# Performance work log

Measured on AMD Instinct MI355X. Metric: run time of the kernel, lower is better.

Reference implementation:

```python
import jax, jax.numpy as jnp
import numpy as np

B, F, T, D, O = 8192, 512, 64, 6, 128
N_INTERNAL = 2 ** D - 1  # 63
N_LEAVES = 2 ** D        # 64


def smooth_step(t):
    tc = jnp.clip(t, -0.5, 0.5)
    return -2.0 * tc ** 3 + 1.5 * tc + 0.5


def setup_inputs() -> dict:
    key = jax.random.key(0)
    k1, k2, k3, k4 = jax.random.split(key, 4)
    x = jax.random.normal(k1, (B, F), dtype=jnp.float32)
    # Stacked per-node Linear weights in BFS (heap) order: node i -> row i.
    W_nodes = jax.random.normal(k2, (N_INTERNAL, F, T), dtype=jnp.float32) * (1.0 / np.sqrt(F))
    b_nodes = jax.random.normal(k3, (N_INTERNAL, T), dtype=jnp.float32) * 0.01
    # Per-leaf mixing weight [out_features, num_trees], leaves in BFS order.
    W_leaf = jax.random.normal(k4, (N_LEAVES, O, T), dtype=jnp.float32)
    return {"x": x, "W_nodes": W_nodes, "b_nodes": b_nodes, "W_leaf": W_leaf}


def reference(x, W_nodes, b_nodes, W_leaf):
    n_internal = W_nodes.shape[0]
    depth = int(np.log2(n_internal + 1))
    # All internal-node gates in one stacked GEMM: [B, n_internal, T]
    s = smooth_step(jnp.einsum('bf,nft->bnt', x, W_nodes) + b_nodes[None, :, :])
    b, _, t = s.shape
    prob = jnp.ones((b, 1, t), dtype=s.dtype)  # root prob
    start = 0
    for lvl in range(depth):
        width = 2 ** lvl
        s_l = s[:, start:start + width]  # [B, width, T], nodes at this level
        start += width
        # node local j -> children local 2j (left, prob*s) and 2j+1 (right, prob*(1-s))
        prob = jnp.stack([prob * s_l, prob * (1.0 - s_l)], axis=2).reshape(b, 2 * width, t)
    # prob: [B, n_leaves, T]; mix per-leaf, per-tree weights -> [B, O]
    out = jnp.einsum('blt,lot->bo', prob, W_leaf)
    return out
```

## Files before the change

kernel.cpp:

```cpp
#include <hip/hip_runtime.h>
#include <hip/hip_fp16.h>

#define BATCH 8192
#define FDIM  512
#define NTREE 64
#define NODES 63
#define ODIM  128
#define NJ    (NODES*NTREE)
#define NJP   4096
#define K2    4096

typedef _Float16 f16;
typedef _Float16 f16x8 __attribute__((ext_vector_type(8)));
typedef float    f32x4 __attribute__((ext_vector_type(4)));

#define XH_OFF   0
#define XH_SZ    ((size_t)BATCH*FDIM*2)
#define WNH_OFF  (XH_OFF + XH_SZ)
#define WNH_SZ   ((size_t)NJP*FDIM*2)
#define WLT_OFF  (WNH_OFF + WNH_SZ)
#define WLT_SZ   ((size_t)ODIM*K2*2)
#define SP_OFF   (WLT_OFF + WLT_SZ)
#define SP_SZ    ((size_t)BATCH*NJP*2)
#define WS_NEEDED (SP_OFF + SP_SZ)

__device__ __forceinline__ float smooth_step_f(float t) {
    float tc = fminf(fmaxf(t, -0.5f), 0.5f);
    return fmaf(tc, fmaf(-2.0f * tc, tc, 1.5f), 0.5f);
}

__device__ __forceinline__ void async16(const void* g, void* l) {
    __builtin_amdgcn_global_load_lds((__attribute__((address_space(1))) void*)g,
                                     (__attribute__((address_space(3))) void*)l,
                                     16, 0, 0);
}

__device__ __forceinline__ int sw_off(int row, int g) {
    return ((row >> 3) * 512) + (((row & 7) * 8 + (g ^ (row & 7))) * 8);
}

__global__ void conv_x_kernel(const float* __restrict__ in, f16* __restrict__ out) {
    size_t i = ((size_t)blockIdx.x * blockDim.x + threadIdx.x) * 4;
    float4 v = *(const float4*)(in + i);
    f16* o = out + i;
    o[0] = (f16)v.x; o[1] = (f16)v.y; o[2] = (f16)v.z; o[3] = (f16)v.w;
}

__global__ void conv_wl_kernel(const float* __restrict__ in, f16* __restrict__ out) {
    const int l  = blockIdx.x;
    const int os = threadIdx.x >> 6;
    const int t  = threadIdx.x & 63;
    for (int oo = 0; oo < 32; ++oo) {
        int o = oo * 4 + os;
        out[(size_t)o * K2 + l * 64 + t] = (f16)in[(size_t)l * (ODIM * NTREE) + o * 64 + t];
    }
}

__global__ void conv_wn_kernel(const float* __restrict__ wn, f16* __restrict__ out) {
    const int n    = blockIdx.x;
    const int f0   = blockIdx.y * 64;
    const int lane = threadIdx.x & 63;
    const int w    = threadIdx.x >> 6;
    if (n == NODES) {
        #pragma unroll
        for (int jj = 0; jj < 16; ++jj) {
            int j = NJ + w * 16 + jj;
            out[(size_t)j * FDIM + f0 + lane] = (f16)0.0f;
        }
        return;
    }
    __shared__ float tile[64][65];
    const float* src = wn + (size_t)n * (FDIM * NTREE);
    #pragma unroll
    for (int i = 0; i < 16; ++i) {
        int fl = w * 16 + i;
        tile[fl][lane] = src[(size_t)(f0 + fl) * NTREE + lane];
    }
    __syncthreads();
    #pragma unroll
    for (int i = 0; i < 16; ++i) {
        int tr = w * 16 + i;
        out[(size_t)(n * 64 + tr) * FDIM + f0 + lane] = (f16)tile[lane][tr];
    }
}

__global__ __launch_bounds__(256, 3)
void gemm_nodes(const f16* __restrict__ xh, const f16* __restrict__ wnh,
                const float* __restrict__ bn, f16* __restrict__ s_out)
{
    __shared__ f16 SH[128 * 128];
    f16* Ash = SH;
    f16* Bsh = SH + 128 * 64;
    const int tid  = threadIdx.x;
    const int lane = tid & 63;
    const int w    = tid >> 6;
    const int wm   = w & 1;
    const int wn   = w >> 1;
    const int j0   = blockIdx.x * 128;
    const int row0 = blockIdx.y * 128;

    const int lr = lane >> 3;
    const int lg = (lane & 7) ^ lr;
    f32x4 acc[4][4] = {};

    for (int k0 = 0; k0 < FDIM; k0 += 64) {
        #pragma unroll
        for (int q = 0; q < 8; ++q) {
            int id = w * 8 + q;
            if (id < 16) {
                int r = id * 8 + lr;
                async16(xh + (size_t)(row0 + r) * FDIM + k0 + lg * 8, &Ash[id * 512 + lane * 8]);
            } else {
                int c = id - 16;
                int r = c * 8 + lr;
                async16(wnh + (size_t)(j0 + r) * FDIM + k0 + lg * 8, &Bsh[c * 512 + lane * 8]);
            }
        }
        __syncthreads();
        #pragma unroll
        for (int ks = 0; ks < 2; ++ks) {
            int g = ks * 4 + (lane >> 4);
            f16x8 bfr[4];
            #pragma unroll
            for (int tn = 0; tn < 4; ++tn) {
                int j = wn * 64 + tn * 16 + (lane & 15);
                bfr[tn] = *(const f16x8*)&Bsh[sw_off(j, g)];
            }
            #pragma unroll
            for (int tm = 0; tm < 4; ++tm) {
                int m = wm * 64 + tm * 16 + (lane & 15);
                f16x8 afr = *(const f16x8*)&Ash[sw_off(m, g)];
                #pragma unroll
                for (int tn = 0; tn < 4; ++tn)
                    acc[tm][tn] = __builtin_amdgcn_mfma_f32_16x16x32_f16(afr, bfr[tn], acc[tm][tn], 0, 0, 0);
            }
        }
        __syncthreads();
    }

    #pragma unroll
    for (int tn = 0; tn < 4; ++tn) {
        int col = wn * 64 + tn * 16 + (lane & 15);
        int j   = j0 + col;
        float bias = (j < NJ) ? bn[j] : 0.0f;
        #pragma unroll
        for (int tm = 0; tm < 4; ++tm) {
            #pragma unroll
            for (int r = 0; r < 4; ++r) {
                int row = wm * 64 + tm * 16 + (lane >> 4) * 4 + r;
                float v = acc[tm][tn][r] + bias;
                int scol = col ^ (((row >> 2) & 3) << 4);
                SH[row * 128 + scol] = (f16)smooth_step_f(v);
            }
        }
    }
    __syncthreads();
    const int4* shv = (const int4*)SH;
    #pragma unroll
    for (int it = 0; it < 8; ++it) {
        int idx = it * 256 + tid;
        int row = idx >> 4, c = idx & 15;
        int src = (row << 4) + (c ^ (((row >> 2) & 3) << 1));
        ((int4*)(s_out + (size_t)(row0 + row) * NJP + j0))[c] = shv[src];
    }
}

__global__ __launch_bounds__(256, 4)
void prob_kernel(f16* sp)
{
    __shared__ f16 stage[4 * 4096];
    const int lane = threadIdx.x & 63;
    const int w    = threadIdx.x >> 6;
    const size_t row = (size_t)blockIdx.x * 4 + w;
    f16* rp = sp + row * NJP;
    f16* L  = stage + w * 4096;

    #pragma unroll
    for (int c = 0; c < 8; ++c)
        async16(rp + c * 512 + lane * 8, L + c * 512 + lane * 8);
    __builtin_amdgcn_s_waitcnt(0);

    float pr[32];
    pr[0] = 1.0f;
    int base = 0;
    #pragma unroll
    for (int lvl = 0; lvl < 5; ++lvl) {
        const int width = 1 << lvl;
        float sl[16];
        #pragma unroll
        for (int i = 0; i < width; ++i)
            sl[i] = (float)L[(base + i) * 64 + lane];
        #pragma unroll
        for (int i = width - 1; i >= 0; --i) {
            float p = pr[i];
            pr[2 * i]     = p * sl[i];
            pr[2 * i + 1] = p * (1.0f - sl[i]);
        }
        base += width;
    }
    #pragma unroll
    for (int i = 0; i < 32; ++i) {
        float s5 = (float)L[(31 + i) * 64 + lane];
        float p  = pr[i];
        L[(2 * i) * 64 + lane]     = (f16)(p * s5);
        L[(2 * i + 1) * 64 + lane] = (f16)(p * (1.0f - s5));
    }
    const int4* ls = (const int4*)L;
    int4* gd = (int4*)rp;
    #pragma unroll
    for (int c = 0; c < 8; ++c)
        gd[c * 64 + lane] = ls[c * 64 + lane];
}

__global__ __launch_bounds__(256, 4)
void leaf_gemm(const f16* __restrict__ prob, const f16* __restrict__ wlt,
               float* __restrict__ out)
{
    __shared__ f16 Ash[2 * 16 * 64];
    __shared__ f16 Bsh[2 * 128 * 64];
    const int tid  = threadIdx.x;
    const int lane = tid & 63;
    const int w    = tid >> 6;
    const int row0 = blockIdx.x * 16;

    const int lr = lane >> 3;
    const int lg = (lane & 7) ^ lr;
    f32x4 acc[2] = {};

    for (int k0 = 0; k0 < K2; k0 += 128) {
        #pragma unroll
        for (int q = 0; q < 9; ++q) {
            int id = w * 9 + q;
            if (id < 4) {
                int t = id >> 1, c = id & 1;
                int r = c * 8 + lr;
                async16(prob + (size_t)(row0 + r) * NJP + k0 + t * 64 + lg * 8,
                        &Ash[t * 1024 + c * 512 + lane * 8]);
            } else {
                int e = id - 4;
                int t = e >> 4, c = e & 15;
                int o = c * 8 + lr;
                async16(wlt + (size_t)o * K2 + k0 + t * 64 + lg * 8,
                        &Bsh[t * 8192 + c * 512 + lane * 8]);
            }
        }
        __syncthreads();
        #pragma unroll
        for (int ks = 0; ks < 4; ++ks) {
            int t = ks >> 1;
            int g = (ks & 1) * 4 + (lane >> 4);
            int m = lane & 15;
            f16x8 afr = *(const f16x8*)&Ash[t * 1024 + sw_off(m, g)];
            #pragma unroll
            for (int tn = 0; tn < 2; ++tn) {
                int o = w * 32 + tn * 16 + (lane & 15);
                f16x8 bfr = *(const f16x8*)&Bsh[t * 8192 + sw_off(o, g)];
                acc[tn] = __builtin_amdgcn_mfma_f32_16x16x32_f16(afr, bfr, acc[tn], 0, 0, 0);
            }
        }
        __syncthreads();
    }
    #pragma unroll
    for (int tn = 0; tn < 2; ++tn) {
        int o = w * 32 + tn * 16 + (lane & 15);
        #pragma unroll
        for (int r = 0; r < 4; ++r) {
            int row = row0 + (lane >> 4) * 4 + r;
            out[(size_t)row * ODIM + o] = acc[tn][r];
        }
    }
}

#define ROWS 8
__global__ __launch_bounds__(256, 2)
void soft_tree_fallback(const float* __restrict__ x, const float* __restrict__ Wn,
                        const float* __restrict__ bn, const float* __restrict__ Wl,
                        float* __restrict__ out)
{
    __shared__ __half s_lds[ROWS][NODES][NTREE];
    const int lane = threadIdx.x & 63;
    const int w    = threadIdx.x >> 6;
    const long row0 = (long)blockIdx.x * ROWS;
    for (int n = w; n < NODES; n += 4) {
        const float* wp = Wn + ((long)n * FDIM) * NTREE + lane;
        const float* xp = x + row0 * FDIM;
        float acc[ROWS];
        #pragma unroll
        for (int r = 0; r < ROWS; ++r) acc[r] = 0.0f;
        #pragma unroll 8
        for (int f = 0; f < FDIM; ++f) {
            float wv = wp[(long)f * NTREE];
            #pragma unroll
            for (int r = 0; r < ROWS; ++r)
                acc[r] = fmaf(xp[r * FDIM + f], wv, acc[r]);
        }
        float bias = bn[n * NTREE + lane];
        #pragma unroll
        for (int r = 0; r < ROWS; ++r)
            s_lds[r][n][lane] = __float2half(smooth_step_f(acc[r] + bias));
    }
    __syncthreads();
    const int r0 = w * 2, r1 = w * 2 + 1;
    float pr0[64], pr1[64];
    {
        pr0[0] = 1.0f; pr1[0] = 1.0f;
        int base = 0;
        #pragma unroll
        for (int lvl = 0; lvl < 6; ++lvl) {
            const int width = 1 << lvl;
            #pragma unroll
            for (int i = width - 1; i >= 0; --i) {
                float sa = __half2float(s_lds[r0][base + i][lane]);
                float sb = __half2float(s_lds[r1][base + i][lane]);
                float pa = pr0[i], pb = pr1[i];
                pr0[2 * i] = pa * sa; pr0[2 * i + 1] = pa * (1.0f - sa);
                pr1[2 * i] = pb * sb; pr1[2 * i + 1] = pb * (1.0f - sb);
            }
            base += width;
        }
    }
    for (int o = 0; o < ODIM; ++o) {
        const float* wlp = Wl + (long)o * NTREE + lane;
        float c0 = 0.0f, c1 = 0.0f;
        #pragma unroll
        for (int l = 0; l < 64; ++l) {
            float wv = wlp[(long)l * (ODIM * NTREE)];
            c0 = fmaf(pr0[l], wv, c0);
            c1 = fmaf(pr1[l], wv, c1);
        }
        #pragma unroll
        for (int off = 32; off > 0; off >>= 1) {
            c0 += __shfl_xor(c0, off, 64);
            c1 += __shfl_xor(c1, off, 64);
        }
        if (lane == 0) {
            out[(row0 + r0) * ODIM + o] = c0;
            out[(row0 + r1) * ODIM + o] = c1;
        }
    }
}

extern "C" void kernel_launch(void* const* d_in, const int* in_sizes, int n_in,
                              void* d_out, int out_size, void* d_ws, size_t ws_size,
                              hipStream_t stream) {
    const float* x  = (const float*)d_in[0];
    const float* Wn = (const float*)d_in[1];
    const float* bn = (const float*)d_in[2];
    const float* Wl = (const float*)d_in[3];
    float* out = (float*)d_out;

    if (ws_size < WS_NEEDED) {
        soft_tree_fallback<<<BATCH / ROWS, 256, 0, stream>>>(x, Wn, bn, Wl, out);
        return;
    }

    f16* xh  = (f16*)((char*)d_ws + XH_OFF);
    f16* wnh = (f16*)((char*)d_ws + WNH_OFF);
    f16* wlt = (f16*)((char*)d_ws + WLT_OFF);
    f16* sp  = (f16*)((char*)d_ws + SP_OFF);

    conv_x_kernel <<<(BATCH * FDIM) / (256 * 4), 256, 0, stream>>>(x, xh);
    conv_wl_kernel<<<64, 256, 0, stream>>>(Wl, wlt);
    conv_wn_kernel<<<dim3(64, FDIM / 64), 256, 0, stream>>>(Wn, wnh);

    gemm_nodes<<<dim3(NJP / 128, BATCH / 128), 256, 0, stream>>>(xh, wnh, bn, sp);
    prob_kernel<<<BATCH / 4, 256, 0, stream>>>(sp);
    leaf_gemm<<<BATCH / 16, 256, 0, stream>>>(sp, wlt, out);
}
```

Before: 177.5 us.

## Store gate columns tree-major so prob and leaf kernels work from registers

Changes the node-weight column order from node-major (n*64+t) to tree-major (t*64+n), so each tree's 63 gates plus one pad are contiguous in the gate buffer. The prob kernel now has each lane load its tree's 64 gates as vector loads into registers and write the leaf probabilities back the same way, with no LDS staging. The leaf weight transpose is rebuilt to match the new K ordering, using an LDS tile and vectorized stores. The leaf GEMM drops its LDS tiles and syncs and reads MFMA fragments straight from global memory, which trades LDS traffic for more uncoalesced global loads and higher register pressure.

```diff
diff --git a/kernel.cpp b/kernel.cpp
--- a/kernel.cpp
+++ b/kernel.cpp
@@ -6,7 +6,6 @@
 #define NTREE 64
 #define NODES 63
 #define ODIM  128
-#define NJ    (NODES*NTREE)
 #define NJP   4096
 #define K2    4096
 
@@ -47,12 +46,25 @@
 }
 
 __global__ void conv_wl_kernel(const float* __restrict__ in, f16* __restrict__ out) {
-    const int l  = blockIdx.x;
-    const int os = threadIdx.x >> 6;
-    const int t  = threadIdx.x & 63;
-    for (int oo = 0; oo < 32; ++oo) {
-        int o = oo * 4 + os;
-        out[(size_t)o * K2 + l * 64 + t] = (f16)in[(size_t)l * (ODIM * NTREE) + o * 64 + t];
+    __shared__ f16 tile[64][72];
+    const int o    = blockIdx.x;
+    const int lane = threadIdx.x & 63;
+    const int w    = threadIdx.x >> 6;
+    #pragma unroll
+    for (int lc = 0; lc < 16; ++lc) {
+        int l = w * 16 + lc;
+        tile[lane][l] = (f16)in[(size_t)l * (ODIM * NTREE) + o * 64 + lane];
+    }
+    __syncthreads();
+    f16* orow = out + (size_t)o * K2;
+    #pragma unroll
+    for (int c = 0; c < 2; ++c) {
+        int idx = (threadIdx.x * 2 + c) * 8;
+        int t = idx >> 6, l = idx & 63;
+        f16x8 v;
+        #pragma unroll
+        for (int e = 0; e < 8; ++e) v[e] = tile[t][l + e];
+        *(f16x8*)(orow + idx) = v;
     }
 }
 
@@ -63,9 +75,9 @@
     const int w    = threadIdx.x >> 6;
     if (n == NODES) {
         #pragma unroll
-        for (int jj = 0; jj < 16; ++jj) {
-            int j = NJ + w * 16 + jj;
-            out[(size_t)j * FDIM + f0 + lane] = (f16)0.0f;
+        for (int tc = 0; tc < 16; ++tc) {
+            int t = w * 16 + tc;
+            out[(size_t)(t * 64 + NODES) * FDIM + f0 + lane] = (f16)0.0f;
         }
         return;
     }
@@ -79,8 +91,8 @@
     __syncthreads();
     #pragma unroll
     for (int i = 0; i < 16; ++i) {
-        int tr = w * 16 + i;
-        out[(size_t)(n * 64 + tr) * FDIM + f0 + lane] = (f16)tile[lane][tr];
+        int t = w * 16 + i;
+        out[(size_t)(t * 64 + n) * FDIM + f0 + lane] = (f16)tile[lane][t];
     }
 }
 
@@ -141,8 +153,9 @@
     #pragma unroll
     for (int tn = 0; tn < 4; ++tn) {
         int col = wn * 64 + tn * 16 + (lane & 15);
-        int j   = j0 + col;
-        float bias = (j < NJ) ? bn[j] : 0.0f;
+        int c   = j0 + col;
+        int nn  = c & 63, tt = c >> 6;
+        float bias = (nn < NODES) ? bn[nn * NTREE + tt] : 0.0f;
         #pragma unroll
         for (int tm = 0; tm < 4; ++tm) {
             #pragma unroll
@@ -165,109 +178,77 @@
     }
 }
 
-__global__ __launch_bounds__(256, 4)
-void prob_kernel(f16* sp)
+__global__ __launch_bounds__(256)
+void prob_kernel(f16* __restrict__ sp)
 {
-    __shared__ f16 stage[4 * 4096];
     const int lane = threadIdx.x & 63;
     const int w    = threadIdx.x >> 6;
     const size_t row = (size_t)blockIdx.x * 4 + w;
-    f16* rp = sp + row * NJP;
-    f16* L  = stage + w * 4096;
-
+    f16* base = sp + row * NJP + lane * 64;
+
+    f16x8 gv[8];
+    #pragma unroll
+    for (int c = 0; c < 8; ++c) gv[c] = ((const f16x8*)base)[c];
+    float g[64];
     #pragma unroll
     for (int c = 0; c < 8; ++c)
-        async16(rp + c * 512 + lane * 8, L + c * 512 + lane * 8);
-    __builtin_amdgcn_s_waitcnt(0);
+        #pragma unroll
+        for (int e = 0; e < 8; ++e) g[c * 8 + e] = (float)gv[c][e];
 
     float pr[32];
     pr[0] = 1.0f;
-    int base = 0;
+    int bse = 0;
     #pragma unroll
     for (int lvl = 0; lvl < 5; ++lvl) {
         const int width = 1 << lvl;
-        float sl[16];
-        #pragma unroll
-        for (int i = 0; i < width; ++i)
-            sl[i] = (float)L[(base + i) * 64 + lane];
         #pragma unroll
         for (int i = width - 1; i >= 0; --i) {
-            float p = pr[i];
-            pr[2 * i]     = p * sl[i];
-            pr[2 * i + 1] = p * (1.0f - sl[i]);
-        }
-        base += width;
-    }
+            float p = pr[i], s = g[bse + i];
+            pr[2 * i]     = p * s;
+            pr[2 * i + 1] = p * (1.0f - s);
+        }
+        bse += width;
+    }
+    f16x8 ov[8];
     #pragma unroll
     for (int i = 0; i < 32; ++i) {
-        float s5 = (float)L[(31 + i) * 64 + lane];
-        float p  = pr[i];
-        L[(2 * i) * 64 + lane]     = (f16)(p * s5);
-        L[(2 * i + 1) * 64 + lane] = (f16)(p * (1.0f - s5));
-    }
-    const int4* ls = (const int4*)L;
-    int4* gd = (int4*)rp;
-    #pragma unroll
-    for (int c = 0; c < 8; ++c)
-        gd[c * 64 + lane] = ls[c * 64 + lane];
-}
-
-__global__ __launch_bounds__(256, 4)
+        float p = pr[i], s = g[31 + i];
+        ov[i >> 2][(i & 3) * 2]     = (f16)(p * s);
+        ov[i >> 2][(i & 3) * 2 + 1] = (f16)(p * (1.0f - s));
+    }
+    #pragma unroll
+    for (int c = 0; c < 8; ++c) ((f16x8*)base)[c] = ov[c];
+}
+
+__global__ __launch_bounds__(256)
 void leaf_gemm(const f16* __restrict__ prob, const f16* __restrict__ wlt,
                float* __restrict__ out)
 {
-    __shared__ f16 Ash[2 * 16 * 64];
-    __shared__ f16 Bsh[2 * 128 * 64];
-    const int tid  = threadIdx.x;
-    const int lane = tid & 63;
-    const int w    = tid >> 6;
+    const int lane = threadIdx.x & 63;
+    const int w    = threadIdx.x >> 6;
     const int row0 = blockIdx.x * 16;
-
-    const int lr = lane >> 3;
-    const int lg = (lane & 7) ^ lr;
+    const int o0   = w * 32;
+    const int m = lane & 15, q = lane >> 4;
+
+    const f16* ap  = prob + (size_t)(row0 + m) * NJP + q * 8;
+    const f16* bp0 = wlt + (size_t)(o0 + m) * K2 + q * 8;
+    const f16* bp1 = bp0 + (size_t)16 * K2;
+
     f32x4 acc[2] = {};
-
-    for (int k0 = 0; k0 < K2; k0 += 128) {
-        #pragma unroll
-        for (int q = 0; q < 9; ++q) {
-            int id = w * 9 + q;
-            if (id < 4) {
-                int t = id >> 1, c = id & 1;
-                int r = c * 8 + lr;
-                async16(prob + (size_t)(row0 + r) * NJP + k0 + t * 64 + lg * 8,
-                        &Ash[t * 1024 + c * 512 + lane * 8]);
-            } else {
-                int e = id - 4;
-                int t = e >> 4, c = e & 15;
-                int o = c * 8 + lr;
-                async16(wlt + (size_t)o * K2 + k0 + t * 64 + lg * 8,
-                        &Bsh[t * 8192 + c * 512 + lane * 8]);
-            }
-        }
-        __syncthreads();
-        #pragma unroll
-        for (int ks = 0; ks < 4; ++ks) {
-            int t = ks >> 1;
-            int g = (ks & 1) * 4 + (lane >> 4);
-            int m = lane & 15;
-            f16x8 afr = *(const f16x8*)&Ash[t * 1024 + sw_off(m, g)];
-            #pragma unroll
-            for (int tn = 0; tn < 2; ++tn) {
-                int o = w * 32 + tn * 16 + (lane & 15);
-                f16x8 bfr = *(const f16x8*)&Bsh[t * 8192 + sw_off(o, g)];
-                acc[tn] = __builtin_amdgcn_mfma_f32_16x16x32_f16(afr, bfr, acc[tn], 0, 0, 0);
-            }
-        }
-        __syncthreads();
+    #pragma unroll 4
+    for (int k = 0; k < K2; k += 32) {
+        f16x8 af  = *(const f16x8*)(ap + k);
+        f16x8 bf0 = *(const f16x8*)(bp0 + k);
+        f16x8 bf1 = *(const f16x8*)(bp1 + k);
+        acc[0] = __builtin_amdgcn_mfma_f32_16x16x32_f16(af, bf0, acc[0], 0, 0, 0);
+        acc[1] = __builtin_amdgcn_mfma_f32_16x16x32_f16(af, bf1, acc[1], 0, 0, 0);
     }
     #pragma unroll
     for (int tn = 0; tn < 2; ++tn) {
-        int o = w * 32 + tn * 16 + (lane & 15);
-        #pragma unroll
-        for (int r = 0; r < 4; ++r) {
-            int row = row0 + (lane >> 4) * 4 + r;
-            out[(size_t)row * ODIM + o] = acc[tn][r];
-        }
+        int o = o0 + tn * 16 + m;
+        #pragma unroll
+        for (int r = 0; r < 4; ++r)
+            out[(size_t)(row0 + q * 4 + r) * ODIM + o] = acc[tn][r];
     }
 }
 
@@ -360,7 +341,7 @@
     f16* sp  = (f16*)((char*)d_ws + SP_OFF);
 
     conv_x_kernel <<<(BATCH * FDIM) / (256 * 4), 256, 0, stream>>>(x, xh);
-    conv_wl_kernel<<<64, 256, 0, stream>>>(Wl, wlt);
+    conv_wl_kernel<<<ODIM, 256, 0, stream>>>(Wl, wlt);
     conv_wn_kernel<<<dim3(64, FDIM / 64), 256, 0, stream>>>(Wn, wnh);
 
     gemm_nodes<<<dim3(NJP / 128, BATCH / 128), 256, 0, stream>>>(xh, wnh, bn, sp);
```

Result: slower. 236.8 us (+33.4%).
